# Optimization experiments

Hardware: AMD Instinct MI355X
Metric: run time of the kernel (lower is better)

## Reference

```python
import jax, jax.numpy as jnp
import numpy as np

N_NODES = 100000
N_EDGES = 1600000
IN_SIZE = 256
HID = 64
HEADS = 2
OUT_SIZE = 16


def _gat_layer(x, W, a_l, a_r, b, src, dst, n_nodes, heads, feat):
    # x: [N, Din]; W: [Din, H*F]; a_l, a_r: [H, F]; b: [H*F]
    h = (x @ W).reshape(n_nodes, heads, feat)          # [N, H, F]
    el = jnp.sum(h * a_l, axis=-1)                     # [N, H]
    er = jnp.sum(h * a_r, axis=-1)                     # [N, H]
    e = jax.nn.leaky_relu(el[src] + er[dst], 0.2)      # [E, H]
    # segment softmax over incoming edges of each dst node
    m = jax.ops.segment_max(e, dst, num_segments=n_nodes)
    m = jnp.where(jnp.isfinite(m), m, 0.0)             # nodes with no in-edges
    p = jnp.exp(e - m[dst])                            # [E, H]
    s = jax.ops.segment_sum(p, dst, num_segments=n_nodes)
    alpha = p / (s[dst] + 1e-9)                        # [E, H]
    # scatter-add weighted source features
    out = jax.ops.segment_sum(alpha[:, :, None] * h[src], dst, num_segments=n_nodes)
    return out + b.reshape(1, heads, feat)             # [N, H, F]


def setup_inputs() -> dict:
    key = jax.random.key(0)
    ks = jax.random.split(key, 12)
    features = jax.random.normal(ks[0], (N_NODES, IN_SIZE), dtype=jnp.float32)
    src = jax.random.randint(ks[1], (N_EDGES,), 0, N_NODES, dtype=jnp.int32)
    dst = jax.random.randint(ks[2], (N_EDGES,), 0, N_NODES, dtype=jnp.int32)
    s1 = 1.0 / np.sqrt(IN_SIZE)
    s2 = 1.0 / np.sqrt(HID * HEADS)
    W1 = jax.random.normal(ks[3], (IN_SIZE, HEADS * HID), dtype=jnp.float32) * s1
    al1 = jax.random.normal(ks[4], (HEADS, HID), dtype=jnp.float32) * 0.1
    ar1 = jax.random.normal(ks[5], (HEADS, HID), dtype=jnp.float32) * 0.1
    b1 = jnp.zeros((HEADS * HID,), dtype=jnp.float32)
    W2 = jax.random.normal(ks[6], (HEADS * HID, HEADS * HID), dtype=jnp.float32) * s2
    al2 = jax.random.normal(ks[7], (HEADS, HID), dtype=jnp.float32) * 0.1
    ar2 = jax.random.normal(ks[8], (HEADS, HID), dtype=jnp.float32) * 0.1
    b2 = jnp.zeros((HEADS * HID,), dtype=jnp.float32)
    Wl = jax.random.normal(ks[9], (HEADS * HID, OUT_SIZE), dtype=jnp.float32) * s2
    bl = jnp.zeros((OUT_SIZE,), dtype=jnp.float32)
    return {"features": features, "src": src, "dst": dst,
            "W1": W1, "al1": al1, "ar1": ar1, "b1": b1,
            "W2": W2, "al2": al2, "ar2": ar2, "b2": b2,
            "Wl": Wl, "bl": bl}


def reference(features, src, dst, W1, al1, ar1, b1, W2, al2, ar2, b2, Wl, bl):
    n = features.shape[0]
    h = _gat_layer(features, W1, al1, ar1, b1.reshape(HEADS, HID).reshape(-1),
                   src, dst, n, HEADS, HID)
    h = jax.nn.elu(h.reshape(n, HEADS * HID))          # flatten(1) + ELU (dropout: eval)
    h = _gat_layer(h, W2, al2, ar2, b2, src, dst, n, HEADS, HID)
    h = jax.nn.elu(h.reshape(n, HEADS * HID))
    return h @ Wl + bl                                  # [N, OUT_SIZE]
```

## Files before the change

### kernel.cpp

```cpp
#include <hip/hip_runtime.h>
#include <hip/hip_fp16.h>

#define N_NODES 100000
#define N_EDGES 1600000
#define IN_SIZE 256
#define HID 64
#define HEADS 2
#define DMODEL 128
#define OUT_SZ 16

#define BSHIFT 7
#define BNODES 128
#define NB 782
#define CAP 4096
#define EPB 2048

typedef _Float16 f16x4 __attribute__((ext_vector_type(4)));
typedef _Float16 f16x8 __attribute__((ext_vector_type(8)));
typedef float f32x4 __attribute__((ext_vector_type(4)));


__global__ __launch_bounds__(256) void bin_kernel(const int* __restrict__ src,
                                                  const int* __restrict__ dst,
                                                  int* __restrict__ counts,
                                                  int2* __restrict__ bucketbuf, int e) {
    __shared__ int hist[NB];
    __shared__ int base[NB];
    int tid = threadIdx.x;
    int start = blockIdx.x * EPB;
    for (int i = tid; i < NB; i += 256) hist[i] = 0;
    __syncthreads();
    int pack[8];
    #pragma unroll
    for (int i = 0; i < 8; i++) {
        int idx = start + i * 256 + tid;
        int p = -1;
        if (idx < e) {
            int b = dst[idx] >> BSHIFT;
            int r = atomicAdd(&hist[b], 1);
            p = (b << 16) | r;
        }
        pack[i] = p;
    }
    __syncthreads();
    for (int i = tid; i < NB; i += 256)
        base[i] = atomicAdd(&counts[i], hist[i]);
    __syncthreads();
    #pragma unroll
    for (int i = 0; i < 8; i++) {
        int idx = start + i * 256 + tid;
        int p = pack[i];
        if (p >= 0) {
            int b = p >> 16;
            int pos = base[b] + (p & 0xffff);
            if (pos < CAP)
                bucketbuf[(size_t)b * CAP + pos] = make_int2(src[idx], dst[idx]);
        }
    }
}

__global__ void bucket_scan_kernel(const int* __restrict__ counts,
                                   int* __restrict__ bases) {
    __shared__ int lds[256];
    int tid = threadIdx.x;
    int c[4];
    int s = 0;
    #pragma unroll
    for (int i = 0; i < 4; i++) {
        int idx = 4 * tid + i;
        c[i] = (idx < NB) ? min(counts[idx], CAP) : 0;
        s += c[i];
    }
    lds[tid] = s;
    __syncthreads();
    for (int off = 1; off < 256; off <<= 1) {
        int x = 0;
        if (tid >= off) x = lds[tid - off];
        __syncthreads();
        lds[tid] += x;
        __syncthreads();
    }
    int run = lds[tid] - s;
    #pragma unroll
    for (int i = 0; i < 4; i++) {
        int idx = 4 * tid + i;
        if (idx < NB) bases[idx] = run;
        run += c[i];
    }
}


__global__ __launch_bounds__(256) void csr_kernel(const int2* __restrict__ bucketbuf,
                                                  const int* __restrict__ counts,
                                                  const int* __restrict__ bases,
                                                  int* __restrict__ deg,
                                                  int* __restrict__ offs,
                                                  int* __restrict__ ssrc, int n) {
    __shared__ int hist[BNODES];
    __shared__ int cursor[BNODES];
    __shared__ int lds[256];
    int b = blockIdx.x;
    int tid = threadIdx.x;
    int cnt = min(counts[b], CAP);
    int base = bases[b];
    int node0 = b << BSHIFT;
    const int2* ebuf = bucketbuf + (size_t)b * CAP;

    if (tid < BNODES) hist[tid] = 0;
    __syncthreads();
    for (int i = tid; i < cnt; i += 256)
        atomicAdd(&hist[ebuf[i].y - node0], 1);
    __syncthreads();

    int h0 = (tid < BNODES) ? hist[tid] : 0;
    lds[tid] = h0;
    __syncthreads();
    for (int off = 1; off < 256; off <<= 1) {
        int x = 0;
        if (tid >= off) x = lds[tid - off];
        __syncthreads();
        lds[tid] += x;
        __syncthreads();
    }
    int excl = lds[tid] - h0;
    if (tid < BNODES) {
        cursor[tid] = excl;
        int g0 = node0 + tid;
        if (g0 < n) { deg[g0] = h0; offs[g0] = base + excl; }
    }
    __syncthreads();

    for (int i = tid; i < cnt; i += 256) {
        int2 ed = ebuf[i];
        int p = atomicAdd(&cursor[ed.y - node0], 1);
        ssrc[base + p] = ed.x;
    }
}


template <int K>
__global__ void wt_kernel(const float* __restrict__ W, _Float16* __restrict__ Wt) {
    int i = blockIdx.x * blockDim.x + threadIdx.x;
    if (i >= 128 * K) return;
    int nr = i / K;
    int k = i - nr * K;
    Wt[i] = (_Float16)W[(size_t)k * 128 + nr];
}


template <int K, bool F16IN>
__global__ __launch_bounds__(256) void gemm_attn_kernel(const void* __restrict__ Ap,
                                                        const _Float16* __restrict__ Wt,
                                                        const float* __restrict__ al,
                                                        const float* __restrict__ ar,
                                                        uint32_t* __restrict__ h16,
                                                        float* __restrict__ el,
                                                        float* __restrict__ er, int n) {
    __shared__ _Float16 As[64 * 72];
    __shared__ _Float16 Bs[128 * 72];
    int tid = threadIdx.x;
    int w = tid >> 6;
    int lane = tid & 63;
    int c = lane & 15;
    int quad = lane >> 4;
    int r0 = blockIdx.x * 64;

    f32x4 acc[8];
    #pragma unroll
    for (int t = 0; t < 8; t++) acc[t] = (f32x4){0.f, 0.f, 0.f, 0.f};

    for (int kt = 0; kt < K; kt += 64) {
        {
            int lr = tid >> 4;
            int lc = (tid & 15) * 4;
            #pragma unroll
            for (int q = 0; q < 4; q++) {
                int row = lr + 16 * q;
                int gr = r0 + row;
                if constexpr (F16IN) {
                    const uint32_t* Af = (const uint32_t*)Ap;
                    uint2 v = make_uint2(0u, 0u);
                    if (gr < n) v = *(const uint2*)(Af + (size_t)gr * (K / 2) + (kt + lc) / 2);
                    *(uint2*)(As + row * 72 + lc) = v;
                } else {
                    const float* Af = (const float*)Ap;
                    float4 v = make_float4(0.f, 0.f, 0.f, 0.f);
                    if (gr < n) v = *(const float4*)(Af + (size_t)gr * K + kt + lc);
                    f16x4 hv = {(_Float16)v.x, (_Float16)v.y, (_Float16)v.z, (_Float16)v.w};
                    *(f16x4*)(As + row * 72 + lc) = hv;
                }
            }
            int nr = tid >> 1;
            int kc = (tid & 1) * 32;
            const uint4* gsrc = (const uint4*)(Wt + (size_t)nr * K + kt + kc);
            uint4 v0 = gsrc[0];
            uint4 v1 = gsrc[1];
            uint4 v2 = gsrc[2];
            uint4 v3 = gsrc[3];
            *(uint4*)(Bs + nr * 72 + kc + 0)  = v0;
            *(uint4*)(Bs + nr * 72 + kc + 8)  = v1;
            *(uint4*)(Bs + nr * 72 + kc + 16) = v2;
            *(uint4*)(Bs + nr * 72 + kc + 24) = v3;
        }
        __syncthreads();

        #pragma unroll
        for (int kk = 0; kk < 64; kk += 32) {
            f16x8 a = *(const f16x8*)(As + (16 * w + c) * 72 + kk + quad * 8);
            #pragma unroll
            for (int t = 0; t < 8; t++) {
                f16x8 b = *(const f16x8*)(Bs + (16 * t + c) * 72 + kk + quad * 8);
                acc[t] = __builtin_amdgcn_mfma_f32_16x16x32_f16(a, b, acc[t], 0, 0, 0);
            }
        }
        __syncthreads();
    }

    #pragma unroll
    for (int i = 0; i < 4; i++) {
        int gr = r0 + 16 * w + quad * 4 + i;
        float el0 = 0.f, el1 = 0.f, er0 = 0.f, er1 = 0.f;
        #pragma unroll
        for (int t = 0; t < 8; t++) {
            float hv = acc[t][i];
            float alv = al[16 * t + c];
            float arv = ar[16 * t + c];
            if (t < 4) { el0 += hv * alv; er0 += hv * arv; }
            else       { el1 += hv * alv; er1 += hv * arv; }
        }
        #pragma unroll
        for (int off = 1; off < 16; off <<= 1) {
            el0 += __shfl_xor(el0, off);
            el1 += __shfl_xor(el1, off);
            er0 += __shfl_xor(er0, off);
            er1 += __shfl_xor(er1, off);
        }
        if (c == 0 && gr < n) {
            *(float2*)(el + 2 * gr) = make_float2(el0, el1);
            *(float2*)(er + 2 * gr) = make_float2(er0, er1);
        }
        #pragma unroll
        for (int t = 0; t < 8; t++) {
            float own = acc[t][i];
            float other = __shfl_xor(own, 1);
            if ((c & 1) == 0 && gr < n) {
                __half2 hh = __floats2half2_rn(own, other);
                h16[(size_t)gr * 64 + 8 * t + (c >> 1)] = *(const uint32_t*)&hh;
            }
        }
    }
}


__device__ __forceinline__ float edge_w(float2 e, float erh, int head) {
    float x = (head ? e.y : e.x) + erh;
    x = x >= 0.f ? x : 0.2f * x;
    return __expf(x);
}

__device__ __forceinline__ void acc8(uint4 u, float w, float* a) {
    union { uint4 u4; f16x8 h8; } cv;
    cv.u4 = u;
    #pragma unroll
    for (int i = 0; i < 8; i++)
        a[i] = fmaf((float)cv.h8[i], w, a[i]);
}

__global__ __launch_bounds__(256) void agg_kernel(const uint32_t* __restrict__ hb,
                                                  const int* __restrict__ ssrc,
                                                  const float* __restrict__ el,
                                                  const float* __restrict__ er,
                                                  const float* __restrict__ bias,
                                                  const int* __restrict__ offs,
                                                  const int* __restrict__ deg,
                                                  uint32_t* __restrict__ out16, int n) {
    int wid = (blockIdx.x * blockDim.x + threadIdx.x) >> 6;
    int lane = threadIdx.x & 63;
    if (wid >= n) return;
    int start = offs[wid];
    int d = deg[wid];
    int g = lane >> 4;
    int fl = lane & 15;
    int head = fl >> 3;

    float2 erv = *(const float2*)(er + 2 * wid);
    float erh = head ? erv.y : erv.x;

    const int* sp = ssrc + start;
    const float2* el2 = (const float2*)el;
    const char* hbb = (const char*)hb;
    uint32_t foff = (uint32_t)(fl << 4);

    float a[8];
    #pragma unroll
    for (int i = 0; i < 8; i++) a[i] = 0.f;
    float psum = 0.f;

    int j = 0;
    if (d >= 16) {
        int s0 = sp[g];
        int s1 = sp[4 + g];
        int s2 = sp[8 + g];
        int s3 = sp[12 + g];
        for (; j + 32 <= d; j += 16) {
            float2 e0 = el2[s0];
            uint4 u0 = *(const uint4*)(hbb + (((uint32_t)s0 << 8) + foff));
            float2 e1 = el2[s1];
            uint4 u1 = *(const uint4*)(hbb + (((uint32_t)s1 << 8) + foff));
            float2 e2 = el2[s2];
            uint4 u2 = *(const uint4*)(hbb + (((uint32_t)s2 << 8) + foff));
            float2 e3 = el2[s3];
            uint4 u3 = *(const uint4*)(hbb + (((uint32_t)s3 << 8) + foff));
            int ns0 = sp[j + 16 + g];
            int ns1 = sp[j + 20 + g];
            int ns2 = sp[j + 24 + g];
            int ns3 = sp[j + 28 + g];
            float w0 = edge_w(e0, erh, head);
            float w1 = edge_w(e1, erh, head);
            float w2 = edge_w(e2, erh, head);
            float w3 = edge_w(e3, erh, head);
            psum += (w0 + w1) + (w2 + w3);
            acc8(u0, w0, a);
            acc8(u1, w1, a);
            acc8(u2, w2, a);
            acc8(u3, w3, a);
            s0 = ns0; s1 = ns1; s2 = ns2; s3 = ns3;
        }
        {
            float2 e0 = el2[s0];
            uint4 u0 = *(const uint4*)(hbb + (((uint32_t)s0 << 8) + foff));
            float2 e1 = el2[s1];
            uint4 u1 = *(const uint4*)(hbb + (((uint32_t)s1 << 8) + foff));
            float2 e2 = el2[s2];
            uint4 u2 = *(const uint4*)(hbb + (((uint32_t)s2 << 8) + foff));
            float2 e3 = el2[s3];
            uint4 u3 = *(const uint4*)(hbb + (((uint32_t)s3 << 8) + foff));
            float w0 = edge_w(e0, erh, head);
            float w1 = edge_w(e1, erh, head);
            float w2 = edge_w(e2, erh, head);
            float w3 = edge_w(e3, erh, head);
            psum += (w0 + w1) + (w2 + w3);
            acc8(u0, w0, a);
            acc8(u1, w1, a);
            acc8(u2, w2, a);
            acc8(u3, w3, a);
            j += 16;
        }
    }
    if (j < d) {
        int last = d - 1;
        int i0 = j + g, i1 = j + 4 + g, i2 = j + 8 + g, i3 = j + 12 + g;
        int s0 = sp[min(i0, last)];
        int s1 = sp[min(i1, last)];
        int s2 = sp[min(i2, last)];
        int s3 = sp[min(i3, last)];
        float2 e0 = el2[s0];
        uint4 u0 = *(const uint4*)(hbb + (((uint32_t)s0 << 8) + foff));
        float2 e1 = el2[s1];
        uint4 u1 = *(const uint4*)(hbb + (((uint32_t)s1 << 8) + foff));
        float2 e2 = el2[s2];
        uint4 u2 = *(const uint4*)(hbb + (((uint32_t)s2 << 8) + foff));
        float2 e3 = el2[s3];
        uint4 u3 = *(const uint4*)(hbb + (((uint32_t)s3 << 8) + foff));
        float w0 = (i0 <= last) ? edge_w(e0, erh, head) : 0.f;
        float w1 = (i1 <= last) ? edge_w(e1, erh, head) : 0.f;
        float w2 = (i2 <= last) ? edge_w(e2, erh, head) : 0.f;
        float w3 = (i3 <= last) ? edge_w(e3, erh, head) : 0.f;
        psum += (w0 + w1) + (w2 + w3);
        acc8(u0, w0, a);
        acc8(u1, w1, a);
        acc8(u2, w2, a);
        acc8(u3, w3, a);
    }

    #pragma unroll
    for (int i = 0; i < 8; i++) {
        a[i] += __shfl_xor(a[i], 16);
        a[i] += __shfl_xor(a[i], 32);
    }
    psum += __shfl_xor(psum, 16);
    psum += __shfl_xor(psum, 32);

    if (lane < 16) {
        float inv = 1.f / (psum + 1e-9f);
        float4 b0 = *(const float4*)(bias + 8 * lane);
        float4 b1 = *(const float4*)(bias + 8 * lane + 4);
        float o[8];
        o[0] = fmaf(a[0], inv, b0.x);
        o[1] = fmaf(a[1], inv, b0.y);
        o[2] = fmaf(a[2], inv, b0.z);
        o[3] = fmaf(a[3], inv, b0.w);
        o[4] = fmaf(a[4], inv, b1.x);
        o[5] = fmaf(a[5], inv, b1.y);
        o[6] = fmaf(a[6], inv, b1.z);
        o[7] = fmaf(a[7], inv, b1.w);
        #pragma unroll
        for (int i = 0; i < 8; i++)
            o[i] = o[i] > 0.f ? o[i] : (__expf(o[i]) - 1.f);
        __half2 h01 = __floats2half2_rn(o[0], o[1]);
        __half2 h23 = __floats2half2_rn(o[2], o[3]);
        __half2 h45 = __floats2half2_rn(o[4], o[5]);
        __half2 h67 = __floats2half2_rn(o[6], o[7]);
        uint4 ov = make_uint4(*(const uint32_t*)&h01, *(const uint32_t*)&h23,
                              *(const uint32_t*)&h45, *(const uint32_t*)&h67);
        ((uint4*)(out16 + (size_t)wid * 64))[lane] = ov;
    }
}


__global__ __launch_bounds__(256) void final_kernel(const uint32_t* __restrict__ x16,
                                                    const float* __restrict__ Wl,
                                                    const float* __restrict__ bl,
                                                    float* __restrict__ out, int n) {
    __shared__ float Ws[DMODEL * OUT_SZ];
    __shared__ float bs[OUT_SZ];
    int tid = threadIdx.x;
    for (int i = tid; i < DMODEL * OUT_SZ / 4; i += 256)
        ((float4*)Ws)[i] = ((const float4*)Wl)[i];
    if (tid < OUT_SZ) bs[tid] = bl[tid];
    __syncthreads();
    int node = blockIdx.x * 16 + (tid >> 4);
    int c = tid & 15;
    if (node >= n) return;
    const uint2* xr = (const uint2*)(x16 + (size_t)node * 64);
    float acc = bs[c];
    #pragma unroll
    for (int kk = 0; kk < 32; kk++) {
        uint2 v = xr[kk];
        float2 f0 = __half22float2(*(const __half2*)&v.x);
        float2 f1 = __half22float2(*(const __half2*)&v.y);
        acc += f0.x * Ws[(4 * kk + 0) * OUT_SZ + c];
        acc += f0.y * Ws[(4 * kk + 1) * OUT_SZ + c];
        acc += f1.x * Ws[(4 * kk + 2) * OUT_SZ + c];
        acc += f1.y * Ws[(4 * kk + 3) * OUT_SZ + c];
    }
    out[(size_t)node * OUT_SZ + c] = acc;
}


extern "C" void kernel_launch(void* const* d_in, const int* in_sizes, int n_in,
                              void* d_out, int out_size, void* d_ws, size_t ws_size,
                              hipStream_t stream) {
    const float* features = (const float*)d_in[0];
    const int*   src      = (const int*)d_in[1];
    const int*   dst      = (const int*)d_in[2];
    const float* W1  = (const float*)d_in[3];
    const float* al1 = (const float*)d_in[4];
    const float* ar1 = (const float*)d_in[5];
    const float* b1  = (const float*)d_in[6];
    const float* W2  = (const float*)d_in[7];
    const float* al2 = (const float*)d_in[8];
    const float* ar2 = (const float*)d_in[9];
    const float* b2  = (const float*)d_in[10];
    const float* Wl  = (const float*)d_in[11];
    const float* bl  = (const float*)d_in[12];
    float* out = (float*)d_out;

    const int n = N_NODES, e = N_EDGES;

    char* w = (char*)d_ws;
    uint32_t* h16 = (uint32_t*)w;       w += (size_t)n * 64 * 4;
    uint32_t* x1  = (uint32_t*)w;       w += (size_t)n * 64 * 4;
    uint32_t* x2  = (uint32_t*)w;       w += 26 * 1024 * 1024;
    float* el   = (float*)w;            w += (size_t)n * 2 * 4;
    float* er   = (float*)w;            w += (size_t)n * 2 * 4;
    int* deg    = (int*)w;              w += 400128;
    int* offs   = (int*)w;              w += 400128;
    int* ssrc   = (int*)w;              w += (size_t)e * 4;
    int* counts = (int*)w;              w += 4096;
    int* bases  = (int*)w;              w += 4096;
    _Float16* Wt1 = (_Float16*)w;       w += 128 * IN_SIZE * 2;
    _Float16* Wt2 = (_Float16*)w;       w += 128 * DMODEL * 2;
    int2* bucketbuf = (int2*)x2;

    const int binBlocks = (e + EPB - 1) / EPB;
    const int gemmBlocks = (n + 63) / 64;
    const int aggBlocks = (n + 3) / 4;
    const int finalBlocks = (n + 15) / 16;

    hipMemsetAsync(counts, 0, NB * 4, stream);
    bin_kernel<<<binBlocks, 256, 0, stream>>>(src, dst, counts, bucketbuf, e);
    bucket_scan_kernel<<<1, 256, 0, stream>>>(counts, bases);
    csr_kernel<<<NB, 256, 0, stream>>>(bucketbuf, counts, bases, deg, offs, ssrc, n);

    wt_kernel<IN_SIZE><<<(128 * IN_SIZE + 255) / 256, 256, 0, stream>>>(W1, Wt1);
    wt_kernel<DMODEL><<<(128 * DMODEL + 255) / 256, 256, 0, stream>>>(W2, Wt2);

    gemm_attn_kernel<IN_SIZE, false><<<gemmBlocks, 256, 0, stream>>>(features, Wt1, al1, ar1,
                                                                     h16, el, er, n);
    agg_kernel<<<aggBlocks, 256, 0, stream>>>(h16, ssrc, el, er, b1, offs, deg, x1, n);

    gemm_attn_kernel<DMODEL, true><<<gemmBlocks, 256, 0, stream>>>(x1, Wt2, al2, ar2,
                                                                   h16, el, er, n);
    agg_kernel<<<aggBlocks, 256, 0, stream>>>(h16, ssrc, el, er, b2, offs, deg, x2, n);

    final_kernel<<<finalBlocks, 256, 0, stream>>>(x2, Wl, bl, out, n);

    (void)in_sizes; (void)n_in; (void)out_size; (void)ws_size;
}
```

Measured before the change: 437.9 us.

## Fuse final linear layer into second aggregation and coarsen CSR buckets

The final 128x16 projection plus bias now runs inside the second aggregation kernel. Each lane multiplies its ELU outputs by Wl and the partial sums are reduced with shuffles, so the fp16 x2 intermediate and one kernel launch are no longer needed. Separately, the CSR build uses 512-node buckets (196 buckets, 4096 edges per bin block), which cuts global atomics and simplifies the bucket scan. The trade-offs are more per-thread work and Wl reads in the aggregation epilogue, plus higher per-bucket capacity pressure with CAP set to 16384.

```diff
diff --git a/kernel.cpp b/kernel.cpp
--- a/kernel.cpp
+++ b/kernel.cpp
@@ -9,11 +9,11 @@
 #define DMODEL 128
 #define OUT_SZ 16
 
-#define BSHIFT 7
-#define BNODES 128
-#define NB 782
-#define CAP 4096
-#define EPB 2048
+#define BSHIFT 9
+#define BNODES 512
+#define NB 196
+#define CAP 16384
+#define EPB 4096
 
 typedef _Float16 f16x4 __attribute__((ext_vector_type(4)));
 typedef _Float16 f16x8 __attribute__((ext_vector_type(8)));
@@ -30,9 +30,9 @@
     int start = blockIdx.x * EPB;
     for (int i = tid; i < NB; i += 256) hist[i] = 0;
     __syncthreads();
-    int pack[8];
-    #pragma unroll
-    for (int i = 0; i < 8; i++) {
+    int pack[16];
+    #pragma unroll
+    for (int i = 0; i < 16; i++) {
         int idx = start + i * 256 + tid;
         int p = -1;
         if (idx < e) {
@@ -47,7 +47,7 @@
         base[i] = atomicAdd(&counts[i], hist[i]);
     __syncthreads();
     #pragma unroll
-    for (int i = 0; i < 8; i++) {
+    for (int i = 0; i < 16; i++) {
         int idx = start + i * 256 + tid;
         int p = pack[i];
         if (p >= 0) {
@@ -63,15 +63,8 @@
                                    int* __restrict__ bases) {
     __shared__ int lds[256];
     int tid = threadIdx.x;
-    int c[4];
-    int s = 0;
-    #pragma unroll
-    for (int i = 0; i < 4; i++) {
-        int idx = 4 * tid + i;
-        c[i] = (idx < NB) ? min(counts[idx], CAP) : 0;
-        s += c[i];
-    }
-    lds[tid] = s;
+    int t = (tid < NB) ? min(counts[tid], CAP) : 0;
+    lds[tid] = t;
     __syncthreads();
     for (int off = 1; off < 256; off <<= 1) {
         int x = 0;
@@ -80,13 +73,7 @@
         lds[tid] += x;
         __syncthreads();
     }
-    int run = lds[tid] - s;
-    #pragma unroll
-    for (int i = 0; i < 4; i++) {
-        int idx = 4 * tid + i;
-        if (idx < NB) bases[idx] = run;
-        run += c[i];
-    }
+    if (tid < NB) bases[tid] = lds[tid] - t;
 }
 
 
@@ -106,14 +93,15 @@
     int node0 = b << BSHIFT;
     const int2* ebuf = bucketbuf + (size_t)b * CAP;
 
-    if (tid < BNODES) hist[tid] = 0;
+    hist[tid] = 0;
+    hist[tid + 256] = 0;
     __syncthreads();
     for (int i = tid; i < cnt; i += 256)
         atomicAdd(&hist[ebuf[i].y - node0], 1);
     __syncthreads();
 
-    int h0 = (tid < BNODES) ? hist[tid] : 0;
-    lds[tid] = h0;
+    int h0 = hist[2 * tid], h1 = hist[2 * tid + 1];
+    lds[tid] = h0 + h1;
     __syncthreads();
     for (int off = 1; off < 256; off <<= 1) {
         int x = 0;
@@ -122,12 +110,12 @@
         lds[tid] += x;
         __syncthreads();
     }
-    int excl = lds[tid] - h0;
-    if (tid < BNODES) {
-        cursor[tid] = excl;
-        int g0 = node0 + tid;
-        if (g0 < n) { deg[g0] = h0; offs[g0] = base + excl; }
-    }
+    int excl = lds[tid] - (h0 + h1);
+    cursor[2 * tid] = excl;
+    cursor[2 * tid + 1] = excl + h0;
+    int g0 = node0 + 2 * tid, g1 = g0 + 1;
+    if (g0 < n) { deg[g0] = h0; offs[g0] = base + excl; }
+    if (g1 < n) { deg[g1] = h1; offs[g1] = base + excl + h0; }
     __syncthreads();
 
     for (int i = tid; i < cnt; i += 256) {
@@ -266,6 +254,7 @@
         a[i] = fmaf((float)cv.h8[i], w, a[i]);
 }
 
+template <bool FUSE_FINAL>
 __global__ __launch_bounds__(256) void agg_kernel(const uint32_t* __restrict__ hb,
                                                   const int* __restrict__ ssrc,
                                                   const float* __restrict__ el,
@@ -273,7 +262,10 @@
                                                   const float* __restrict__ bias,
                                                   const int* __restrict__ offs,
                                                   const int* __restrict__ deg,
-                                                  uint32_t* __restrict__ out16, int n) {
+                                                  uint32_t* __restrict__ out16,
+                                                  const float* __restrict__ Wl,
+                                                  const float* __restrict__ bl,
+                                                  float* __restrict__ outf, int n) {
     int wid = (blockIdx.x * blockDim.x + threadIdx.x) >> 6;
     int lane = threadIdx.x & 63;
     if (wid >= n) return;
@@ -381,60 +373,56 @@
     psum += __shfl_xor(psum, 16);
     psum += __shfl_xor(psum, 32);
 
-    if (lane < 16) {
-        float inv = 1.f / (psum + 1e-9f);
-        float4 b0 = *(const float4*)(bias + 8 * lane);
-        float4 b1 = *(const float4*)(bias + 8 * lane + 4);
-        float o[8];
-        o[0] = fmaf(a[0], inv, b0.x);
-        o[1] = fmaf(a[1], inv, b0.y);
-        o[2] = fmaf(a[2], inv, b0.z);
-        o[3] = fmaf(a[3], inv, b0.w);
-        o[4] = fmaf(a[4], inv, b1.x);
-        o[5] = fmaf(a[5], inv, b1.y);
-        o[6] = fmaf(a[6], inv, b1.z);
-        o[7] = fmaf(a[7], inv, b1.w);
-        #pragma unroll
-        for (int i = 0; i < 8; i++)
-            o[i] = o[i] > 0.f ? o[i] : (__expf(o[i]) - 1.f);
-        __half2 h01 = __floats2half2_rn(o[0], o[1]);
-        __half2 h23 = __floats2half2_rn(o[2], o[3]);
-        __half2 h45 = __floats2half2_rn(o[4], o[5]);
-        __half2 h67 = __floats2half2_rn(o[6], o[7]);
-        uint4 ov = make_uint4(*(const uint32_t*)&h01, *(const uint32_t*)&h23,
-                              *(const uint32_t*)&h45, *(const uint32_t*)&h67);
-        ((uint4*)(out16 + (size_t)wid * 64))[lane] = ov;
-    }
-}
-
-
-__global__ __launch_bounds__(256) void final_kernel(const uint32_t* __restrict__ x16,
-                                                    const float* __restrict__ Wl,
-                                                    const float* __restrict__ bl,
-                                                    float* __restrict__ out, int n) {
-    __shared__ float Ws[DMODEL * OUT_SZ];
-    __shared__ float bs[OUT_SZ];
-    int tid = threadIdx.x;
-    for (int i = tid; i < DMODEL * OUT_SZ / 4; i += 256)
-        ((float4*)Ws)[i] = ((const float4*)Wl)[i];
-    if (tid < OUT_SZ) bs[tid] = bl[tid];
-    __syncthreads();
-    int node = blockIdx.x * 16 + (tid >> 4);
-    int c = tid & 15;
-    if (node >= n) return;
-    const uint2* xr = (const uint2*)(x16 + (size_t)node * 64);
-    float acc = bs[c];
-    #pragma unroll
-    for (int kk = 0; kk < 32; kk++) {
-        uint2 v = xr[kk];
-        float2 f0 = __half22float2(*(const __half2*)&v.x);
-        float2 f1 = __half22float2(*(const __half2*)&v.y);
-        acc += f0.x * Ws[(4 * kk + 0) * OUT_SZ + c];
-        acc += f0.y * Ws[(4 * kk + 1) * OUT_SZ + c];
-        acc += f1.x * Ws[(4 * kk + 2) * OUT_SZ + c];
-        acc += f1.y * Ws[(4 * kk + 3) * OUT_SZ + c];
-    }
-    out[(size_t)node * OUT_SZ + c] = acc;
+    float inv = 1.f / (psum + 1e-9f);
+    float4 b0 = *(const float4*)(bias + 8 * fl);
+    float4 b1 = *(const float4*)(bias + 8 * fl + 4);
+    float o[8];
+    o[0] = fmaf(a[0], inv, b0.x);
+    o[1] = fmaf(a[1], inv, b0.y);
+    o[2] = fmaf(a[2], inv, b0.z);
+    o[3] = fmaf(a[3], inv, b0.w);
+    o[4] = fmaf(a[4], inv, b1.x);
+    o[5] = fmaf(a[5], inv, b1.y);
+    o[6] = fmaf(a[6], inv, b1.z);
+    o[7] = fmaf(a[7], inv, b1.w);
+    #pragma unroll
+    for (int i = 0; i < 8; i++)
+        o[i] = o[i] > 0.f ? o[i] : (__expf(o[i]) - 1.f);
+
+    if constexpr (!FUSE_FINAL) {
+        if (lane < 16) {
+            __half2 h01 = __floats2half2_rn(o[0], o[1]);
+            __half2 h23 = __floats2half2_rn(o[2], o[3]);
+            __half2 h45 = __floats2half2_rn(o[4], o[5]);
+            __half2 h67 = __floats2half2_rn(o[6], o[7]);
+            uint4 ov = make_uint4(*(const uint32_t*)&h01, *(const uint32_t*)&h23,
+                                  *(const uint32_t*)&h45, *(const uint32_t*)&h67);
+            ((uint4*)(out16 + (size_t)wid * 64))[lane] = ov;
+        }
+    } else {
+        const float4* Wl4 = (const float4*)Wl;
+        float p0 = 0.f, p1 = 0.f, p2 = 0.f, p3 = 0.f;
+        #pragma unroll
+        for (int i = 0; i < 8; i++) {
+            float4 wv = Wl4[(8 * fl + i) * 4 + g];
+            p0 = fmaf(o[i], wv.x, p0);
+            p1 = fmaf(o[i], wv.y, p1);
+            p2 = fmaf(o[i], wv.z, p2);
+            p3 = fmaf(o[i], wv.w, p3);
+        }
+        #pragma unroll
+        for (int off = 1; off < 16; off <<= 1) {
+            p0 += __shfl_xor(p0, off);
+            p1 += __shfl_xor(p1, off);
+            p2 += __shfl_xor(p2, off);
+            p3 += __shfl_xor(p3, off);
+        }
+        if (fl == 0) {
+            float4 blv = ((const float4*)bl)[g];
+            float4 ov = make_float4(p0 + blv.x, p1 + blv.y, p2 + blv.z, p3 + blv.w);
+            *(float4*)(outf + (size_t)wid * OUT_SZ + 4 * g) = ov;
+        }
+    }
 }
 
 
@@ -461,22 +449,22 @@
     char* w = (char*)d_ws;
     uint32_t* h16 = (uint32_t*)w;       w += (size_t)n * 64 * 4;
     uint32_t* x1  = (uint32_t*)w;       w += (size_t)n * 64 * 4;
-    uint32_t* x2  = (uint32_t*)w;       w += 26 * 1024 * 1024;
+    char* bbuf    = w;                  w += 26 * 1024 * 1024;
     float* el   = (float*)w;            w += (size_t)n * 2 * 4;
     float* er   = (float*)w;            w += (size_t)n * 2 * 4;
     int* deg    = (int*)w;              w += 400128;
     int* offs   = (int*)w;              w += 400128;
     int* ssrc   = (int*)w;              w += (size_t)e * 4;
-    int* counts = (int*)w;              w += 4096;
-    int* bases  = (int*)w;              w += 4096;
+    int* counts = (int*)w;              w += 1024;
+    int* bases  = (int*)w;              w += 1024;
     _Float16* Wt1 = (_Float16*)w;       w += 128 * IN_SIZE * 2;
     _Float16* Wt2 = (_Float16*)w;       w += 128 * DMODEL * 2;
-    int2* bucketbuf = (int2*)x2;
+    int2* bucketbuf = (int2*)bbuf;
 
     const int binBlocks = (e + EPB - 1) / EPB;
     const int gemmBlocks = (n + 63) / 64;
     const int aggBlocks = (n + 3) / 4;
-    const int finalBlocks = (n + 15) / 16;
+    (void)out_size;
 
     hipMemsetAsync(counts, 0, NB * 4, stream);
     bin_kernel<<<binBlocks, 256, 0, stream>>>(src, dst, counts, bucketbuf, e);
@@ -488,13 +476,13 @@
 
     gemm_attn_kernel<IN_SIZE, false><<<gemmBlocks, 256, 0, stream>>>(features, Wt1, al1, ar1,
                                                                      h16, el, er, n);
-    agg_kernel<<<aggBlocks, 256, 0, stream>>>(h16, ssrc, el, er, b1, offs, deg, x1, n);
+    agg_kernel<false><<<aggBlocks, 256, 0, stream>>>(h16, ssrc, el, er, b1, offs, deg,
+                                                     x1, nullptr, nullptr, nullptr, n);
 
     gemm_attn_kernel<DMODEL, true><<<gemmBlocks, 256, 0, stream>>>(x1, Wt2, al2, ar2,
                                                                    h16, el, er, n);
-    agg_kernel<<<aggBlocks, 256, 0, stream>>>(h16, ssrc, el, er, b2, offs, deg, x2, n);
-
-    final_kernel<<<finalBlocks, 256, 0, stream>>>(x2, Wl, bl, out, n);
-
-    (void)in_sizes; (void)n_in; (void)out_size; (void)ws_size;
-}
+    agg_kernel<true><<<aggBlocks, 256, 0, stream>>>(h16, ssrc, el, er, b2, offs, deg,
+                                                    nullptr, Wl, bl, out, n);
+
+    (void)in_sizes; (void)n_in; (void)ws_size;
+}
```

New measurement: 488.0 us. +11.5%, slower.

## Coarsen CSR buckets and fuse scan, memset and weight transposes into fewer launches

Applied to the files above, without the earlier changes.

Bucket granularity grows from 128 to 512 destination nodes, with larger per-bucket capacity and more edges per bin block. The global bucket prefix scan now runs inside each csr block, which removes the separate scan kernel. Zeroing the counters and both weight transposes move into one fused kernel, which removes the memset and a launch. The aim is to cut launch and serialization overhead in preprocessing, at the cost of fewer csr blocks (196, fewer than the CUs) and more LDS atomic contention per bin.

```diff
diff --git a/kernel.cpp b/kernel.cpp
--- a/kernel.cpp
+++ b/kernel.cpp
@@ -9,15 +9,38 @@
 #define DMODEL 128
 #define OUT_SZ 16
 
-#define BSHIFT 7
-#define BNODES 128
-#define NB 782
-#define CAP 4096
-#define EPB 2048
+#define BSHIFT 9
+#define BNODES 512
+#define NB 196
+#define CAP 16384
+#define EPB 4096
 
 typedef _Float16 f16x4 __attribute__((ext_vector_type(4)));
 typedef _Float16 f16x8 __attribute__((ext_vector_type(8)));
 typedef float f32x4 __attribute__((ext_vector_type(4)));
+
+
+__global__ __launch_bounds__(256) void wt_fused_kernel(const float* __restrict__ W1,
+                                                       _Float16* __restrict__ Wt1,
+                                                       const float* __restrict__ W2,
+                                                       _Float16* __restrict__ Wt2,
+                                                       int* __restrict__ counts) {
+    int tid = threadIdx.x;
+    if (blockIdx.x == 0 && tid < NB) counts[tid] = 0;
+    int i = blockIdx.x * 256 + tid;
+    if (i < 128 * IN_SIZE) {
+        int nr = i / IN_SIZE;
+        int k = i - nr * IN_SIZE;
+        Wt1[i] = (_Float16)W1[(size_t)k * 128 + nr];
+    } else {
+        int j = i - 128 * IN_SIZE;
+        if (j < 128 * DMODEL) {
+            int nr = j / DMODEL;
+            int k = j - nr * DMODEL;
+            Wt2[j] = (_Float16)W2[(size_t)k * 128 + nr];
+        }
+    }
+}
 
 
 __global__ __launch_bounds__(256) void bin_kernel(const int* __restrict__ src,
@@ -30,9 +53,9 @@
     int start = blockIdx.x * EPB;
     for (int i = tid; i < NB; i += 256) hist[i] = 0;
     __syncthreads();
-    int pack[8];
-    #pragma unroll
-    for (int i = 0; i < 8; i++) {
+    int pack[16];
+    #pragma unroll
+    for (int i = 0; i < 16; i++) {
         int idx = start + i * 256 + tid;
         int p = -1;
         if (idx < e) {
@@ -47,7 +70,7 @@
         base[i] = atomicAdd(&counts[i], hist[i]);
     __syncthreads();
     #pragma unroll
-    for (int i = 0; i < 8; i++) {
+    for (int i = 0; i < 16; i++) {
         int idx = start + i * 256 + tid;
         int p = pack[i];
         if (p >= 0) {
@@ -59,40 +82,9 @@
     }
 }
 
-__global__ void bucket_scan_kernel(const int* __restrict__ counts,
-                                   int* __restrict__ bases) {
-    __shared__ int lds[256];
-    int tid = threadIdx.x;
-    int c[4];
-    int s = 0;
-    #pragma unroll
-    for (int i = 0; i < 4; i++) {
-        int idx = 4 * tid + i;
-        c[i] = (idx < NB) ? min(counts[idx], CAP) : 0;
-        s += c[i];
-    }
-    lds[tid] = s;
-    __syncthreads();
-    for (int off = 1; off < 256; off <<= 1) {
-        int x = 0;
-        if (tid >= off) x = lds[tid - off];
-        __syncthreads();
-        lds[tid] += x;
-        __syncthreads();
-    }
-    int run = lds[tid] - s;
-    #pragma unroll
-    for (int i = 0; i < 4; i++) {
-        int idx = 4 * tid + i;
-        if (idx < NB) bases[idx] = run;
-        run += c[i];
-    }
-}
-
 
 __global__ __launch_bounds__(256) void csr_kernel(const int2* __restrict__ bucketbuf,
                                                   const int* __restrict__ counts,
-                                                  const int* __restrict__ bases,
                                                   int* __restrict__ deg,
                                                   int* __restrict__ offs,
                                                   int* __restrict__ ssrc, int n) {
@@ -101,19 +93,9 @@
     __shared__ int lds[256];
     int b = blockIdx.x;
     int tid = threadIdx.x;
-    int cnt = min(counts[b], CAP);
-    int base = bases[b];
-    int node0 = b << BSHIFT;
-    const int2* ebuf = bucketbuf + (size_t)b * CAP;
-
-    if (tid < BNODES) hist[tid] = 0;
-    __syncthreads();
-    for (int i = tid; i < cnt; i += 256)
-        atomicAdd(&hist[ebuf[i].y - node0], 1);
-    __syncthreads();
-
-    int h0 = (tid < BNODES) ? hist[tid] : 0;
-    lds[tid] = h0;
+
+    int t = (tid < NB) ? min(counts[tid], CAP) : 0;
+    lds[tid] = t;
     __syncthreads();
     for (int off = 1; off < 256; off <<= 1) {
         int x = 0;
@@ -122,12 +104,36 @@
         lds[tid] += x;
         __syncthreads();
     }
-    int excl = lds[tid] - h0;
-    if (tid < BNODES) {
-        cursor[tid] = excl;
-        int g0 = node0 + tid;
-        if (g0 < n) { deg[g0] = h0; offs[g0] = base + excl; }
-    }
+    int base = (b == 0) ? 0 : lds[b - 1];
+    int cnt = min(counts[b], CAP);
+    __syncthreads();
+
+    int node0 = b << BSHIFT;
+    const int2* ebuf = bucketbuf + (size_t)b * CAP;
+
+    hist[tid] = 0;
+    hist[tid + 256] = 0;
+    __syncthreads();
+    for (int i = tid; i < cnt; i += 256)
+        atomicAdd(&hist[ebuf[i].y - node0], 1);
+    __syncthreads();
+
+    int h0 = hist[2 * tid], h1 = hist[2 * tid + 1];
+    lds[tid] = h0 + h1;
+    __syncthreads();
+    for (int off = 1; off < 256; off <<= 1) {
+        int x = 0;
+        if (tid >= off) x = lds[tid - off];
+        __syncthreads();
+        lds[tid] += x;
+        __syncthreads();
+    }
+    int excl = lds[tid] - (h0 + h1);
+    cursor[2 * tid] = excl;
+    cursor[2 * tid + 1] = excl + h0;
+    int g0 = node0 + 2 * tid, g1 = g0 + 1;
+    if (g0 < n) { deg[g0] = h0; offs[g0] = base + excl; }
+    if (g1 < n) { deg[g1] = h1; offs[g1] = base + excl + h0; }
     __syncthreads();
 
     for (int i = tid; i < cnt; i += 256) {
@@ -135,16 +141,6 @@
         int p = atomicAdd(&cursor[ed.y - node0], 1);
         ssrc[base + p] = ed.x;
     }
-}
-
-
-template <int K>
-__global__ void wt_kernel(const float* __restrict__ W, _Float16* __restrict__ Wt) {
-    int i = blockIdx.x * blockDim.x + threadIdx.x;
-    if (i >= 128 * K) return;
-    int nr = i / K;
-    int k = i - nr * K;
-    Wt[i] = (_Float16)W[(size_t)k * 128 + nr];
 }
 
 
@@ -467,24 +463,21 @@
     int* deg    = (int*)w;              w += 400128;
     int* offs   = (int*)w;              w += 400128;
     int* ssrc   = (int*)w;              w += (size_t)e * 4;
-    int* counts = (int*)w;              w += 4096;
-    int* bases  = (int*)w;              w += 4096;
+    int* counts = (int*)w;              w += 1024;
     _Float16* Wt1 = (_Float16*)w;       w += 128 * IN_SIZE * 2;
     _Float16* Wt2 = (_Float16*)w;       w += 128 * DMODEL * 2;
     int2* bucketbuf = (int2*)x2;
 
     const int binBlocks = (e + EPB - 1) / EPB;
+    const int wtBlocks = (128 * IN_SIZE + 128 * DMODEL + 255) / 256;
     const int gemmBlocks = (n + 63) / 64;
     const int aggBlocks = (n + 3) / 4;
     const int finalBlocks = (n + 15) / 16;
 
-    hipMemsetAsync(counts, 0, NB * 4, stream);
+    wt_fused_kernel<<<wtBlocks, 256, 0, stream>>>(W1, Wt1, W2, Wt2, counts);
+
     bin_kernel<<<binBlocks, 256, 0, stream>>>(src, dst, counts, bucketbuf, e);
-    bucket_scan_kernel<<<1, 256, 0, stream>>>(counts, bases);
-    csr_kernel<<<NB, 256, 0, stream>>>(bucketbuf, counts, bases, deg, offs, ssrc, n);
-
-    wt_kernel<IN_SIZE><<<(128 * IN_SIZE + 255) / 256, 256, 0, stream>>>(W1, Wt1);
-    wt_kernel<DMODEL><<<(128 * DMODEL + 255) / 256, 256, 0, stream>>>(W2, Wt2);
+    csr_kernel<<<NB, 256, 0, stream>>>(bucketbuf, counts, deg, offs, ssrc, n);
 
     gemm_attn_kernel<IN_SIZE, false><<<gemmBlocks, 256, 0, stream>>>(features, Wt1, al1, ar1,
                                                                      h16, el, er, n);
```

Result: faster. 421.5 us (-3.7%).
